# Optimization experiments

Hardware: AMD Instinct MI355X
Metric: run time of the kernel (lower is better)

The kernel has to match this reference:

```python
import jax, jax.numpy as jnp
import numpy as np

B, Q, HIST, HID, NH, D, BS, NBLK, NUMB = 8, 512, 1536, 4096, 32, 128, 64, 32, 256


def _rope(x, pos):
    # GPT-NeoX-style rotary used by Falcon: rotate_half over full head_dim.
    Dh = x.shape[-1]
    inv = 1.0 / (10000.0 ** (jnp.arange(0, Dh, 2, dtype=jnp.float32) / Dh))  # [D/2]
    ang = pos.astype(jnp.float32)[:, None] * inv[None, :]                    # [T, D/2]
    cos = jnp.concatenate([jnp.cos(ang), jnp.cos(ang)], -1)[None, :, None, :]
    sin = jnp.concatenate([jnp.sin(ang), jnp.sin(ang)], -1)[None, :, None, :]
    half = Dh // 2
    rot = jnp.concatenate([-x[..., half:], x[..., :half]], -1)
    return x * cos + rot * sin


def setup_inputs() -> dict:
    key = jax.random.key(0)
    ks = jax.random.split(key, 6)
    hidden_states = jax.random.normal(ks[0], (1, B * Q, HID), jnp.float32) * 0.02
    qkv_weight = jax.random.normal(ks[1], ((NH + 2) * D, HID), jnp.float32) * 0.02
    dense_weight = jax.random.normal(ks[2], (HID, NH * D), jnp.float32) * 0.02
    past_key = jax.random.normal(ks[3], (NUMB, BS, 1, D), jnp.float32) * 0.02
    past_value = jax.random.normal(ks[4], (NUMB, BS, 1, D), jnp.float32) * 0.02
    q_start_loc = (jnp.arange(B) * Q).astype(jnp.int32)
    q_seq_length = jnp.full((B,), Q, jnp.int32)
    history_lengths = jnp.full((B,), HIST, jnp.int32)
    # each sequence owns NBLK distinct cache blocks (shuffled block table)
    block_offsets = jax.random.permutation(ks[5], NUMB).reshape(B, NBLK).astype(jnp.int32)
    position_ids_1d = (history_lengths[:, None] + jnp.arange(Q, dtype=jnp.int32)[None, :]).reshape(-1)
    return dict(hidden_states=hidden_states, qkv_weight=qkv_weight, dense_weight=dense_weight,
                past_key=past_key, past_value=past_value, q_start_loc=q_start_loc,
                q_seq_length=q_seq_length, history_lengths=history_lengths,
                block_offsets=block_offsets, position_ids_1d=position_ids_1d)


def reference(hidden_states, qkv_weight, dense_weight, past_key, past_value,
              q_start_loc, q_seq_length, history_lengths, block_offsets, position_ids_1d):
    T = hidden_states.shape[1]
    Bn = block_offsets.shape[0]
    Qn = T // Bn
    Dh = past_key.shape[-1]
    BSz = past_key.shape[1]
    # fused QKV projection
    fused = hidden_states @ qkv_weight.T                      # [1, T, (NH+2)*D]
    NHh = fused.shape[-1] // Dh - 2
    qkv = fused.reshape(1, T, NHh + 2, Dh)
    q = qkv[:, :, :NHh]                                       # [1, T, NH, D]
    k = qkv[:, :, NHh:NHh + 1]                                 # [1, T, 1, D]
    v = qkv[:, :, NHh + 1:]                                    # [1, T, 1, D]
    # inline rotary embedding on q, k
    q = _rope(q, position_ids_1d)
    k = _rope(k, position_ids_1d)
    # fill_kv_cache: scatter new K/V into paged cache via block table
    seq_id = jnp.repeat(jnp.arange(Bn), Qn)                   # [T]
    pos = position_ids_1d.astype(jnp.int32)                   # absolute kv position
    blk = block_offsets[seq_id, pos // BSz]                   # [T] physical block id
    off = pos % BSz
    past_key = past_key.at[blk, off].set(k.reshape(T, 1, Dh))
    past_value = past_value.at[blk, off].set(v.reshape(T, 1, Dh))
    # paged_attention_fwd: gather per-sequence K/V from paged cache
    KVc = block_offsets.shape[1] * BSz                        # kv capacity == kv_len here
    kseq = past_key[block_offsets].reshape(Bn, KVc, Dh)       # [B, KV, D] (1 kv head squeezed)
    vseq = past_value[block_offsets].reshape(Bn, KVc, Dh)
    qb = q.reshape(Bn, Qn, NHh, Dh)
    scale = 1.0 / jnp.sqrt(jnp.float32(Dh))
    scores = jnp.einsum('bqhd,bkd->bhqk', qb, kseq) * scale   # [B, H, Q, KV]
    qpos = history_lengths[:, None] + jnp.arange(Qn)[None, :] # [B, Q]
    mask = jnp.arange(KVc)[None, None, :] <= qpos[:, :, None] # causal + length mask
    scores = jnp.where(mask[:, None, :, :], scores, jnp.float32(-1e30))
    attn = jax.nn.softmax(scores, axis=-1)
    out = jnp.einsum('bhqk,bkd->bqhd', attn, vseq)            # [B, Q, H, D]
    out = out.reshape(1, T, NHh * Dh)
    return out @ dense_weight.T                                # [1, T, hidden]
```

## Files before the change

### kernel.cpp

```cpp
#include <hip/hip_runtime.h>

typedef __attribute__((ext_vector_type(8))) short bf16x8;
typedef __attribute__((ext_vector_type(4))) float f32x4;
typedef __attribute__((ext_vector_type(16))) float f32x16;
typedef __attribute__((ext_vector_type(2))) unsigned int u32x2;

constexpr int B_ = 8, Q_ = 512, HIST_ = 1536, HID_ = 4096, NH_ = 32, D_ = 128;
constexpr int BS_ = 64, NBLK_ = 32;
constexpr int T_ = B_ * Q_;
constexpr int QKVN = (NH_ + 2) * D_;
constexpr int KVC = NBLK_ * BS_;

__device__ __forceinline__ unsigned short f2bf(float f) {
  union { float f; unsigned u; } v; v.f = f;
  unsigned r = v.u + 0x7FFFu + ((v.u >> 16) & 1u);
  return (unsigned short)(r >> 16);
}
__device__ __forceinline__ float bf2f(unsigned short s) {
  union { unsigned u; float f; } v; v.u = ((unsigned)s) << 16;
  return v.f;
}
__device__ __forceinline__ int cvtpk_bf16(float lo, float hi) {
  int r;
  asm("v_cvt_pk_bf16_f32 %0, %1, %2" : "=v"(r) : "v"(lo), "v"(hi));
  return r;
}

__global__ void k_conv3(const float* __restrict__ a, unsigned short* __restrict__ oa, int na,
                        const float* __restrict__ b2, unsigned short* __restrict__ ob, int nb,
                        const float* __restrict__ c3, unsigned short* __restrict__ oc, int nc) {
  int i = blockIdx.x * blockDim.x + threadIdx.x;
  const int stride = gridDim.x * blockDim.x;
  const int tot = na + nb + nc;
  for (; i < tot; i += stride) {
    const float* src; unsigned short* dst; int j = i;
    if (j < na) { src = a; dst = oa; }
    else if ((j -= na) < nb) { src = b2; dst = ob; }
    else { j -= nb; src = c3; dst = oc; }
    float4 v = reinterpret_cast<const float4*>(src)[j];
    ushort4 o;
    o.x = f2bf(v.x); o.y = f2bf(v.y); o.z = f2bf(v.z); o.w = f2bf(v.w);
    reinterpret_cast<ushort4*>(dst)[j] = o;
  }
}

#define LDA4(af, cur_, qq)                                                              \
  {                                                                                     \
    const unsigned short* a_t = sA + (cur_) * 16384;                                    \
    const int r0 = wr * 128 + (qq) * 32 + lr;                                           \
    const int r1 = r0 + 16;                                                             \
    af[0][0] = *(const bf16x8*)&a_t[r0 * 64 + ((lk ^ (r0 & 7)) << 3)];                  \
    af[0][1] = *(const bf16x8*)&a_t[r0 * 64 + (((4 + lk) ^ (r0 & 7)) << 3)];            \
    af[1][0] = *(const bf16x8*)&a_t[r1 * 64 + ((lk ^ (r1 & 7)) << 3)];                  \
    af[1][1] = *(const bf16x8*)&a_t[r1 * 64 + (((4 + lk) ^ (r1 & 7)) << 3)];            \
  }

#define LDB2(dst, cur_, nn)                                                             \
  {                                                                                     \
    const unsigned short* b_t = sB + (cur_) * 16384;                                    \
    const int rb = wc * 64 + (nn) * 16 + lr;                                            \
    dst[nn][0] = *(const bf16x8*)&b_t[rb * 64 + ((lk ^ (rb & 7)) << 3)];                \
    dst[nn][1] = *(const bf16x8*)&b_t[rb * 64 + (((4 + lk) ^ (rb & 7)) << 3)];          \
  }

#define MFMA16(qq, af, Bf)                                                              \
  __builtin_amdgcn_s_setprio(1);                                                        \
  acc[(qq)*2+0][0] = __builtin_amdgcn_mfma_f32_16x16x32_bf16(af[0][0], Bf[0][0], acc[(qq)*2+0][0], 0, 0, 0); \
  acc[(qq)*2+0][1] = __builtin_amdgcn_mfma_f32_16x16x32_bf16(af[0][0], Bf[1][0], acc[(qq)*2+0][1], 0, 0, 0); \
  acc[(qq)*2+0][2] = __builtin_amdgcn_mfma_f32_16x16x32_bf16(af[0][0], Bf[2][0], acc[(qq)*2+0][2], 0, 0, 0); \
  acc[(qq)*2+0][3] = __builtin_amdgcn_mfma_f32_16x16x32_bf16(af[0][0], Bf[3][0], acc[(qq)*2+0][3], 0, 0, 0); \
  acc[(qq)*2+1][0] = __builtin_amdgcn_mfma_f32_16x16x32_bf16(af[1][0], Bf[0][0], acc[(qq)*2+1][0], 0, 0, 0); \
  acc[(qq)*2+1][1] = __builtin_amdgcn_mfma_f32_16x16x32_bf16(af[1][0], Bf[1][0], acc[(qq)*2+1][1], 0, 0, 0); \
  acc[(qq)*2+1][2] = __builtin_amdgcn_mfma_f32_16x16x32_bf16(af[1][0], Bf[2][0], acc[(qq)*2+1][2], 0, 0, 0); \
  acc[(qq)*2+1][3] = __builtin_amdgcn_mfma_f32_16x16x32_bf16(af[1][0], Bf[3][0], acc[(qq)*2+1][3], 0, 0, 0); \
  acc[(qq)*2+0][0] = __builtin_amdgcn_mfma_f32_16x16x32_bf16(af[0][1], Bf[0][1], acc[(qq)*2+0][0], 0, 0, 0); \
  acc[(qq)*2+0][1] = __builtin_amdgcn_mfma_f32_16x16x32_bf16(af[0][1], Bf[1][1], acc[(qq)*2+0][1], 0, 0, 0); \
  acc[(qq)*2+0][2] = __builtin_amdgcn_mfma_f32_16x16x32_bf16(af[0][1], Bf[2][1], acc[(qq)*2+0][2], 0, 0, 0); \
  acc[(qq)*2+0][3] = __builtin_amdgcn_mfma_f32_16x16x32_bf16(af[0][1], Bf[3][1], acc[(qq)*2+0][3], 0, 0, 0); \
  acc[(qq)*2+1][0] = __builtin_amdgcn_mfma_f32_16x16x32_bf16(af[1][1], Bf[0][1], acc[(qq)*2+1][0], 0, 0, 0); \
  acc[(qq)*2+1][1] = __builtin_amdgcn_mfma_f32_16x16x32_bf16(af[1][1], Bf[1][1], acc[(qq)*2+1][1], 0, 0, 0); \
  acc[(qq)*2+1][2] = __builtin_amdgcn_mfma_f32_16x16x32_bf16(af[1][1], Bf[2][1], acc[(qq)*2+1][2], 0, 0, 0); \
  acc[(qq)*2+1][3] = __builtin_amdgcn_mfma_f32_16x16x32_bf16(af[1][1], Bf[3][1], acc[(qq)*2+1][3], 0, 0, 0); \
  __builtin_amdgcn_s_setprio(0);

#define SYNCPT                                                                          \
  asm volatile("s_waitcnt vmcnt(4)" ::: "memory");                                      \
  __builtin_amdgcn_s_barrier();                                                         \
  asm volatile("" ::: "memory");

#define TILE(t_, cur_, BCUR, BNEXT)                                                     \
  {                                                                                     \
    bf16x8 af[2][2];                                                                    \
    LDA4(af, cur_, 0);                                                                  \
    stage(A, m0, sA, (t_) + 1, 0);                                                      \
    MFMA16(0, af, BCUR);                                                                \
    LDA4(af, cur_, 1);                                                                  \
    stage(A, m0, sA, (t_) + 1, 1);                                                      \
    MFMA16(1, af, BCUR);                                                                \
    SYNCPT;                                                                             \
    LDA4(af, cur_, 2);                                                                  \
    LDB2(BNEXT, (cur_) ^ 1, 0); LDB2(BNEXT, (cur_) ^ 1, 1);                             \
    stage(Bm, n0, sB, (t_) + 2, 0);                                                     \
    MFMA16(2, af, BCUR);                                                                \
    LDA4(af, cur_, 3);                                                                  \
    LDB2(BNEXT, (cur_) ^ 1, 2); LDB2(BNEXT, (cur_) ^ 1, 3);                             \
    stage(Bm, n0, sB, (t_) + 2, 1);                                                     \
    MFMA16(3, af, BCUR);                                                                \
    SYNCPT;                                                                             \
  }

__global__ __launch_bounds__(512, 2) void k_gemm256(const unsigned short* __restrict__ A,
                          const unsigned short* __restrict__ Bm,
                          float* __restrict__ Cf, unsigned short* __restrict__ Cb,
                          int MB, int K, int ldc) {
  extern __shared__ unsigned short smem[];
  unsigned short* sA = smem;
  unsigned short* sB = smem + 32768;
  const int tid = threadIdx.x, lane = tid & 63, w = tid >> 6;
  const int wr = w >> 2, wc = w & 3;
  const int lr = lane & 15, lk = lane >> 4;

  const int nwg = gridDim.x, orig = blockIdx.x;
  const int q8 = nwg >> 3, r8 = nwg & 7, xcd = orig & 7;
  const int wg = (xcd < r8 ? xcd * (q8 + 1) : r8 * (q8 + 1) + (xcd - r8) * q8) + (orig >> 3);
  const int m0 = (wg % MB) * 256;
  const int n0 = (wg / MB) * 256;
  const int NT = K >> 6;

  f32x4 acc[8][4];
#pragma unroll
  for (int mf = 0; mf < 8; ++mf)
#pragma unroll
    for (int nf = 0; nf < 4; ++nf) acc[mf][nf] = f32x4{0.f, 0.f, 0.f, 0.f};

  auto stage = [&](const unsigned short* __restrict__ Mat, int rbase, unsigned short* regionBase,
                   int ts, int half) {
    const int di = ts < NT ? ts : NT - 1;
    const size_t k0 = (size_t)di << 6;
    char* hb = (char*)(regionBase + (ts & 1) * 16384 + half * 8192);
#pragma unroll
    for (int c = 0; c < 2; ++c) {
      const int ob = c * 8192 + (w << 10) + (lane << 4);
      const int row = ob >> 7;
      const int sl = ((ob >> 4) & 7) ^ (row & 7);
      const unsigned short* src = Mat + (size_t)(rbase + half * 128 + row) * K + k0 + sl * 8;
      __builtin_amdgcn_global_load_lds((const __attribute__((address_space(1))) void*)src,
          (__attribute__((address_space(3))) void*)(hb + c * 8192 + (w << 10)), 16, 0, 0);
    }
  };

  stage(A, m0, sA, 0, 0); stage(A, m0, sA, 0, 1);
  stage(Bm, n0, sB, 0, 0); stage(Bm, n0, sB, 0, 1);
  stage(Bm, n0, sB, 1, 0); stage(Bm, n0, sB, 1, 1);
  asm volatile("s_waitcnt vmcnt(4)" ::: "memory");
  __builtin_amdgcn_s_barrier();
  asm volatile("" ::: "memory");
  bf16x8 bX[4][2], bY[4][2];
  LDB2(bX, 0, 0); LDB2(bX, 0, 1); LDB2(bX, 0, 2); LDB2(bX, 0, 3);

  for (int t = 0; t < NT; t += 2) {
    TILE(t, 0, bX, bY)
    TILE(t + 1, 1, bY, bX)
  }
  asm volatile("s_waitcnt vmcnt(0)" ::: "memory");

#pragma unroll
  for (int mf = 0; mf < 8; ++mf)
#pragma unroll
    for (int nf = 0; nf < 4; ++nf)
#pragma unroll
      for (int j = 0; j < 4; ++j) {
        const int rr = m0 + wr * 128 + mf * 16 + lk * 4 + j;
        const int cc = n0 + wc * 64 + nf * 16 + lr;
        if (Cb) Cb[(size_t)rr * ldc + cc] = f2bf(acc[mf][nf][j]);
        else Cf[(size_t)rr * ldc + cc] = acc[mf][nf][j];
      }
}

__global__ void k_rope(const unsigned short* __restrict__ fused,
                       const int* __restrict__ pos_ids,
                       unsigned short* __restrict__ qb,
                       unsigned short* __restrict__ kseq,
                       unsigned short* __restrict__ vtg) {
  int t = blockIdx.x;
  int d = threadIdx.x;
  int b = t >> 9, q = t & 511;
  int pos = pos_ids[t];
  __shared__ float cs[64], sn[64];
  if (d < 64) {
    float inv = powf(10000.f, -(float)d * (1.f / 64.f));
    float ang = (float)pos * inv;
    cs[d] = cosf(ang);
    sn[d] = sinf(ang);
  }
  __syncthreads();
  const float scale = 0.1275174313836907f;
  float c = cs[d & 63], s = sn[d & 63];
  const unsigned short* row = fused + (size_t)t * QKVN;
#pragma unroll 4
  for (int h = 0; h < NH_; ++h) {
    float x = bf2f(row[h * D_ + d]);
    float xr = (d < 64) ? -bf2f(row[h * D_ + d + 64]) : bf2f(row[h * D_ + d - 64]);
    qb[(((size_t)(b * NH_ + h)) * Q_ + q) * D_ + d] = f2bf((x * c + xr * s) * scale);
  }
  {
    float x = bf2f(row[NH_ * D_ + d]);
    float xr = (d < 64) ? -bf2f(row[NH_ * D_ + d + 64]) : bf2f(row[NH_ * D_ + d - 64]);
    kseq[((size_t)b * KVC + pos) * D_ + d] = f2bf(x * c + xr * s);
  }
  vtg[((size_t)b * D_ + d) * KVC + pos] = row[(NH_ + 1) * D_ + d];
}

__global__ void k_gather(const float* __restrict__ pk, const float* __restrict__ pv,
                         const int* __restrict__ bo,
                         unsigned short* __restrict__ kseq, unsigned short* __restrict__ vtg) {
  __shared__ unsigned short vl[64 * 140];
  const int ptile = blockIdx.x;
  const int b = ptile / (HIST_ / 64);
  const int p0 = (ptile % (HIST_ / 64)) * 64;
  const int tid = threadIdx.x;
  const int blk = bo[b * NBLK_ + (p0 >> 6)];
#pragma unroll
  for (int c = 0; c < 8; ++c) {
    int u = c * 256 + tid;
    int p = u >> 5, d4 = u & 31;
    size_t src = ((size_t)blk * BS_ + p) * D_ + d4 * 4;
    float4 kv = *reinterpret_cast<const float4*>(pk + src);
    ushort4 ko;
    ko.x = f2bf(kv.x); ko.y = f2bf(kv.y); ko.z = f2bf(kv.z); ko.w = f2bf(kv.w);
    *reinterpret_cast<ushort4*>(kseq + ((size_t)b * KVC + p0 + p) * D_ + d4 * 4) = ko;
    float4 vv = *reinterpret_cast<const float4*>(pv + src);
    ushort4 vo;
    vo.x = f2bf(vv.x); vo.y = f2bf(vv.y); vo.z = f2bf(vv.z); vo.w = f2bf(vv.w);
    *reinterpret_cast<ushort4*>(&vl[p * 140 + d4 * 4]) = vo;
  }
  __syncthreads();
#pragma unroll
  for (int c = 0; c < 4; ++c) {
    int u = c * 256 + tid;
    int d = u >> 3, pg = u & 7;
    bf16x8 vv8;
#pragma unroll
    for (int i = 0; i < 8; ++i) vv8[i] = (short)vl[(pg * 8 + i) * 140 + d];
    *reinterpret_cast<bf16x8*>(vtg + ((size_t)b * D_ + d) * KVC + p0 + pg * 8) = vv8;
  }
}

__global__ __launch_bounds__(512, 2) void k_attn(const unsigned short* __restrict__ qb,
                       const unsigned short* __restrict__ kseq,
                       const unsigned short* __restrict__ vtg,
                       const int* __restrict__ histL,
                       unsigned short* __restrict__ outb) {
  __shared__ alignas(16) unsigned short kl[2][64 * 128];
  __shared__ alignas(16) unsigned short vt[2][128 * 64];
  const int qt = blockIdx.x, hp = blockIdx.y, b = blockIdx.z;
  const int tid = threadIdx.x, lane = tid & 63, w = tid >> 6;
  const int H = lane >> 5, q = lane & 31;
  const int h = hp * 8 + w;
  const int q0 = qt * 32;
  const int hist = histL[b];
  const unsigned short* kseq_b = kseq + (size_t)b * KVC * D_;
  const unsigned short* vtg_b  = vtg + (size_t)b * D_ * KVC;

  const unsigned short* qrow = qb + (((size_t)(b * NH_ + h)) * Q_ + q0 + q) * D_;
  bf16x8 aq[8];
#pragma unroll
  for (int ds = 0; ds < 8; ++ds)
    aq[ds] = *reinterpret_cast<const bf16x8*>(qrow + ds * 16 + H * 8);

  f32x16 o[4];
#pragma unroll
  for (int db = 0; db < 4; ++db)
#pragma unroll
    for (int r = 0; r < 16; ++r) o[db][r] = 0.f;
  float m = -1e30f, l = 0.f;

  const int ntiles = (hist + q0 + 32 + 63) >> 6;

  auto STAGE = [&](int bufi, int kv0) {
#pragma unroll
    for (int c = 0; c < 2; ++c) {
      int ob = c * 8192 + tid * 16;
      int row = ob >> 8;
      int sp = (ob >> 4) & 15;
      const unsigned short* src = kseq_b + (size_t)(kv0 + row) * D_ + (((sp ^ (row & 15)) << 3));
      __builtin_amdgcn_global_load_lds((const __attribute__((address_space(1))) void*)src,
          (__attribute__((address_space(3))) void*)(&kl[bufi][c * 4096 + w * 512]), 16, 0, 0);
    }
#pragma unroll
    for (int c = 0; c < 2; ++c) {
      int ob = c * 8192 + tid * 16;
      int row = ob >> 7;
      int sp = (ob >> 4) & 7;
      const unsigned short* src = vtg_b + (size_t)row * KVC + kv0 + (((sp ^ (row & 7)) << 3));
      __builtin_amdgcn_global_load_lds((const __attribute__((address_space(1))) void*)src,
          (__attribute__((address_space(3))) void*)(&vt[bufi][c * 4096 + w * 512]), 16, 0, 0);
    }
  };

  STAGE(0, 0);
  __syncthreads();

  for (int it = 0; it < ntiles; ++it) {
    const int cur = it & 1;
    if (it + 1 < ntiles) STAGE(cur ^ 1, (it + 1) * 64);
    const unsigned short* kb = kl[cur];
    const unsigned short* vb = vt[cur];

    f32x16 s0 = f32x16{0.f,0.f,0.f,0.f,0.f,0.f,0.f,0.f,0.f,0.f,0.f,0.f,0.f,0.f,0.f,0.f};
    f32x16 s1 = s0;
#pragma unroll
    for (int ds = 0; ds < 8; ++ds) {
      const int sl = ((2 * ds + H) ^ (q & 15)) << 3;
      bf16x8 k0 = *reinterpret_cast<const bf16x8*>(kb + q * 128 + sl);
      bf16x8 k1 = *reinterpret_cast<const bf16x8*>(kb + (32 + q) * 128 + sl);
      s0 = __builtin_amdgcn_mfma_f32_32x32x16_bf16(k0, aq[ds], s0, 0, 0, 0);
      s1 = __builtin_amdgcn_mfma_f32_32x32x16_bf16(k1, aq[ds], s1, 0, 0, 0);
    }

    if (it == ntiles - 1) {
      const int limit = hist + q0 + q - it * 64 - 4 * H;
#pragma unroll
      for (int r = 0; r < 16; ++r) {
        const int koff = (r & 3) + 8 * ((r >> 2) & 1) + 16 * (r >> 3);
        if (koff > limit) s0[r] = -1e30f;
        if (32 + koff > limit) s1[r] = -1e30f;
      }
    }

    float px[8];
#pragma unroll
    for (int j = 0; j < 8; ++j) {
      float t01 = fmaxf(s0[2 * j], s0[2 * j + 1]);
      px[j] = fmaxf(fmaxf(t01, s1[2 * j]), s1[2 * j + 1]);
    }
    float pa = fmaxf(fmaxf(px[0], px[1]), px[2]);
    float pb2 = fmaxf(fmaxf(px[3], px[4]), px[5]);
    float pmax = fmaxf(fmaxf(pa, pb2), fmaxf(px[6], px[7]));
    pmax = fmaxf(pmax, __shfl_xor(pmax, 32));
    if (__any(pmax > m + 11.54f)) {
      float mn = fmaxf(m, pmax);
      float al = exp2f(m - mn);
      m = mn;
      l *= al;
#pragma unroll
      for (int db = 0; db < 4; ++db)
#pragma unroll
        for (int r = 0; r < 16; ++r) o[db][r] *= al;
    }
#pragma unroll
    for (int r = 0; r < 16; ++r) s0[r] = exp2f(s0[r] - m);
#pragma unroll
    for (int r = 0; r < 16; ++r) s1[r] = exp2f(s1[r] - m);
    float rsum[8];
#pragma unroll
    for (int j = 0; j < 8; ++j)
      rsum[j] = (s0[2 * j] + s0[2 * j + 1]) + (s1[2 * j] + s1[2 * j + 1]);
    float rs = ((rsum[0] + rsum[1]) + (rsum[2] + rsum[3])) + ((rsum[4] + rsum[5]) + (rsum[6] + rsum[7]));
    rs += __shfl_xor(rs, 32);
    l += rs;

#pragma unroll
    for (int s = 0; s < 4; ++s) {
      float p0, p1, p2, p3, p4, p5, p6, p7;
      if (s == 0)      { p0=s0[0];p1=s0[1];p2=s0[2];p3=s0[3];p4=s0[4];p5=s0[5];p6=s0[6];p7=s0[7]; }
      else if (s == 1) { p0=s0[8];p1=s0[9];p2=s0[10];p3=s0[11];p4=s0[12];p5=s0[13];p6=s0[14];p7=s0[15]; }
      else if (s == 2) { p0=s1[0];p1=s1[1];p2=s1[2];p3=s1[3];p4=s1[4];p5=s1[5];p6=s1[6];p7=s1[7]; }
      else             { p0=s1[8];p1=s1[9];p2=s1[10];p3=s1[11];p4=s1[12];p5=s1[13];p6=s1[14];p7=s1[15]; }
      int c01 = cvtpk_bf16(p0, p1);
      int c23 = cvtpk_bf16(p2, p3);
      int c45 = cvtpk_bf16(p4, p5);
      int c67 = cvtpk_bf16(p6, p7);
      u32x2 rA = __builtin_amdgcn_permlane32_swap(c01, c45, false, false);
      u32x2 rB = __builtin_amdgcn_permlane32_swap(c23, c67, false, false);
      union { unsigned wds[4]; bf16x8 v; } uu;
      uu.wds[0] = rA[0]; uu.wds[1] = rB[0]; uu.wds[2] = rA[1]; uu.wds[3] = rB[1];
#pragma unroll
      for (int db = 0; db < 4; ++db) {
        const int row = db * 32 + q;
        bf16x8 vf = *reinterpret_cast<const bf16x8*>(vb + row * 64 + ((((2 * s + H) ^ (row & 7))) << 3));
        o[db] = __builtin_amdgcn_mfma_f32_32x32x16_bf16(vf, uu.v, o[db], 0, 0, 0);
      }
    }
    __syncthreads();
  }

  const float il = 1.f / l;
  unsigned short* orow = outb + (size_t)(b * Q_ + q0 + q) * (NH_ * D_) + h * D_;
#pragma unroll
  for (int db = 0; db < 4; ++db)
#pragma unroll
    for (int rr = 0; rr < 4; ++rr) {
      ushort4 st;
      st.x = f2bf(o[db][rr * 4 + 0] * il);
      st.y = f2bf(o[db][rr * 4 + 1] * il);
      st.z = f2bf(o[db][rr * 4 + 2] * il);
      st.w = f2bf(o[db][rr * 4 + 3] * il);
      *reinterpret_cast<ushort4*>(orow + db * 32 + rr * 8 + 4 * H) = st;
    }
}

extern "C" void kernel_launch(void* const* d_in, const int* in_sizes, int n_in,
                              void* d_out, int out_size, void* d_ws, size_t ws_size,
                              hipStream_t stream) {
  const float* hidden = (const float*)d_in[0];
  const float* qkvw   = (const float*)d_in[1];
  const float* densew = (const float*)d_in[2];
  const float* pk     = (const float*)d_in[3];
  const float* pv     = (const float*)d_in[4];
  const int* histL    = (const int*)d_in[7];
  const int* bo       = (const int*)d_in[8];
  const int* posids   = (const int*)d_in[9];
  float* out = (float*)d_out;

  char* ws = (char*)d_ws;
  unsigned short* ws_hidden = (unsigned short*)(ws);
  unsigned short* ws_wq     = (unsigned short*)(ws + 33554432);
  unsigned short* ws_wd     = (unsigned short*)(ws + 69206016);
  unsigned short* ws_fused  = (unsigned short*)(ws + 102760448);
  unsigned short* ws_q      = (unsigned short*)(ws + 138412032);
  unsigned short* ws_k      = (unsigned short*)(ws + 171966464);
  unsigned short* ws_vt     = (unsigned short*)(ws + 176160768);
  unsigned short* ws_attn   = ws_hidden;

  k_conv3<<<2048, 256, 0, stream>>>(hidden, ws_hidden, T_ * HID_ / 4,
                                    qkvw, ws_wq, QKVN * HID_ / 4,
                                    densew, ws_wd, HID_ * HID_ / 4);
  k_gemm256<<<dim3((T_ / 256) * (QKVN / 256)), 512, 131072, stream>>>(
      ws_hidden, ws_wq, nullptr, ws_fused, T_ / 256, HID_, QKVN);
  k_rope<<<T_, 128, 0, stream>>>(ws_fused, posids, ws_q, ws_k, ws_vt);
  k_gather<<<B_ * (HIST_ / 64), 256, 0, stream>>>(pk, pv, bo, ws_k, ws_vt);
  dim3 ga(Q_ / 32, NH_ / 8, B_);
  k_attn<<<ga, 512, 0, stream>>>(ws_q, ws_k, ws_vt, histL, ws_attn);
  k_gemm256<<<dim3((T_ / 256) * (HID_ / 256)), 512, 131072, stream>>>(
      ws_attn, ws_wd, out, nullptr, T_ / 256, HID_, HID_);
}
```

Baseline: 539.2 us.

## Fuse query RoPE into attention prologue and precompute cos/sin table

Removes the separate rotated-Q buffer by applying rotary embedding and the softmax scale to Q inside the attention kernel as it loads Q from the fused QKV output. A new small kernel precomputes per-token cos/sin tables, used by both the K rope kernel and attention. This removes a full write and re-read of the Q tensor, at the cost of strided Q loads from the fused buffer and extra prologue math and table reads in attention.

```diff
diff --git a/kernel.cpp b/kernel.cpp
--- a/kernel.cpp
+++ b/kernel.cpp
@@ -42,6 +42,14 @@
     o.x = f2bf(v.x); o.y = f2bf(v.y); o.z = f2bf(v.z); o.w = f2bf(v.w);
     reinterpret_cast<ushort4*>(dst)[j] = o;
   }
+}
+
+__global__ void k_tab(const int* __restrict__ posids, float* __restrict__ cs, float* __restrict__ sn) {
+  const int t = blockIdx.x, d = threadIdx.x;
+  const float inv = powf(10000.f, -(float)d * (1.f / 64.f));
+  const float ang = (float)posids[t] * inv;
+  cs[t * 64 + d] = cosf(ang);
+  sn[t * 64 + d] = sinf(ang);
 }
 
 #define LDA4(af, cur_, qq)                                                              \
@@ -177,37 +185,20 @@
       }
 }
 
-__global__ void k_rope(const unsigned short* __restrict__ fused,
-                       const int* __restrict__ pos_ids,
-                       unsigned short* __restrict__ qb,
-                       unsigned short* __restrict__ kseq,
-                       unsigned short* __restrict__ vtg) {
-  int t = blockIdx.x;
-  int d = threadIdx.x;
-  int b = t >> 9, q = t & 511;
-  int pos = pos_ids[t];
-  __shared__ float cs[64], sn[64];
-  if (d < 64) {
-    float inv = powf(10000.f, -(float)d * (1.f / 64.f));
-    float ang = (float)pos * inv;
-    cs[d] = cosf(ang);
-    sn[d] = sinf(ang);
-  }
-  __syncthreads();
-  const float scale = 0.1275174313836907f;
-  float c = cs[d & 63], s = sn[d & 63];
+__global__ void k_ropekv(const unsigned short* __restrict__ fused,
+                         const int* __restrict__ pos_ids,
+                         const float* __restrict__ csT, const float* __restrict__ snT,
+                         unsigned short* __restrict__ kseq,
+                         unsigned short* __restrict__ vtg) {
+  const int t = blockIdx.x;
+  const int d = threadIdx.x;
+  const int b = t >> 9;
+  const int pos = pos_ids[t];
+  const float c = csT[t * 64 + (d & 63)], s = snT[t * 64 + (d & 63)];
   const unsigned short* row = fused + (size_t)t * QKVN;
-#pragma unroll 4
-  for (int h = 0; h < NH_; ++h) {
-    float x = bf2f(row[h * D_ + d]);
-    float xr = (d < 64) ? -bf2f(row[h * D_ + d + 64]) : bf2f(row[h * D_ + d - 64]);
-    qb[(((size_t)(b * NH_ + h)) * Q_ + q) * D_ + d] = f2bf((x * c + xr * s) * scale);
-  }
-  {
-    float x = bf2f(row[NH_ * D_ + d]);
-    float xr = (d < 64) ? -bf2f(row[NH_ * D_ + d + 64]) : bf2f(row[NH_ * D_ + d - 64]);
-    kseq[((size_t)b * KVC + pos) * D_ + d] = f2bf(x * c + xr * s);
-  }
+  const float x = bf2f(row[NH_ * D_ + d]);
+  const float xr = (d < 64) ? -bf2f(row[NH_ * D_ + d + 64]) : bf2f(row[NH_ * D_ + d - 64]);
+  kseq[((size_t)b * KVC + pos) * D_ + d] = f2bf(x * c + xr * s);
   vtg[((size_t)b * D_ + d) * KVC + pos] = row[(NH_ + 1) * D_ + d];
 }
 
@@ -246,7 +237,8 @@
   }
 }
 
-__global__ __launch_bounds__(512, 2) void k_attn(const unsigned short* __restrict__ qb,
+__global__ __launch_bounds__(512, 2) void k_attn(const unsigned short* __restrict__ fused,
+                       const float* __restrict__ csT, const float* __restrict__ snT,
                        const unsigned short* __restrict__ kseq,
                        const unsigned short* __restrict__ vtg,
                        const int* __restrict__ histL,
@@ -262,11 +254,36 @@
   const unsigned short* kseq_b = kseq + (size_t)b * KVC * D_;
   const unsigned short* vtg_b  = vtg + (size_t)b * D_ * KVC;
 
-  const unsigned short* qrow = qb + (((size_t)(b * NH_ + h)) * Q_ + q0 + q) * D_;
+  const int trow = b * Q_ + q0 + q;
+  const unsigned short* qrow = fused + (size_t)trow * QKVN + h * D_;
+  const float* csr = csT + trow * 64;
+  const float* snr = snT + trow * 64;
   bf16x8 aq[8];
 #pragma unroll
   for (int ds = 0; ds < 8; ++ds)
     aq[ds] = *reinterpret_cast<const bf16x8*>(qrow + ds * 16 + H * 8);
+  {
+    const float qsc = 0.1275174313836907f;
+#pragma unroll
+    for (int ds = 0; ds < 4; ++ds) {
+      const int dh0 = ds * 16 + H * 8;
+      float4 ca = *reinterpret_cast<const float4*>(csr + dh0);
+      float4 cb = *reinterpret_cast<const float4*>(csr + dh0 + 4);
+      float4 sa = *reinterpret_cast<const float4*>(snr + dh0);
+      float4 sb = *reinterpret_cast<const float4*>(snr + dh0 + 4);
+      const float cl[8] = {ca.x, ca.y, ca.z, ca.w, cb.x, cb.y, cb.z, cb.w};
+      const float sl[8] = {sa.x, sa.y, sa.z, sa.w, sb.x, sb.y, sb.z, sb.w};
+      bf16x8 lo = aq[ds], hi = aq[ds + 4];
+#pragma unroll
+      for (int j = 0; j < 8; ++j) {
+        const float xl = bf2f((unsigned short)lo[j]);
+        const float xh = bf2f((unsigned short)hi[j]);
+        lo[j] = (short)f2bf((xl * cl[j] - xh * sl[j]) * qsc);
+        hi[j] = (short)f2bf((xh * cl[j] + xl * sl[j]) * qsc);
+      }
+      aq[ds] = lo; aq[ds + 4] = hi;
+    }
+  }
 
   f32x16 o[4];
 #pragma unroll
@@ -418,20 +435,22 @@
   unsigned short* ws_wq     = (unsigned short*)(ws + 33554432);
   unsigned short* ws_wd     = (unsigned short*)(ws + 69206016);
   unsigned short* ws_fused  = (unsigned short*)(ws + 102760448);
-  unsigned short* ws_q      = (unsigned short*)(ws + 138412032);
-  unsigned short* ws_k      = (unsigned short*)(ws + 171966464);
-  unsigned short* ws_vt     = (unsigned short*)(ws + 176160768);
+  float* ws_cs              = (float*)(ws + 138412032);
+  float* ws_sn              = (float*)(ws + 139460608);
+  unsigned short* ws_k      = (unsigned short*)(ws + 140509184);
+  unsigned short* ws_vt     = (unsigned short*)(ws + 144703488);
   unsigned short* ws_attn   = ws_hidden;
 
   k_conv3<<<2048, 256, 0, stream>>>(hidden, ws_hidden, T_ * HID_ / 4,
                                     qkvw, ws_wq, QKVN * HID_ / 4,
                                     densew, ws_wd, HID_ * HID_ / 4);
+  k_tab<<<T_, 64, 0, stream>>>(posids, ws_cs, ws_sn);
   k_gemm256<<<dim3((T_ / 256) * (QKVN / 256)), 512, 131072, stream>>>(
       ws_hidden, ws_wq, nullptr, ws_fused, T_ / 256, HID_, QKVN);
-  k_rope<<<T_, 128, 0, stream>>>(ws_fused, posids, ws_q, ws_k, ws_vt);
+  k_ropekv<<<T_, 128, 0, stream>>>(ws_fused, posids, ws_cs, ws_sn, ws_k, ws_vt);
   k_gather<<<B_ * (HIST_ / 64), 256, 0, stream>>>(pk, pv, bo, ws_k, ws_vt);
   dim3 ga(Q_ / 32, NH_ / 8, B_);
-  k_attn<<<ga, 512, 0, stream>>>(ws_q, ws_k, ws_vt, histL, ws_attn);
+  k_attn<<<ga, 512, 0, stream>>>(ws_fused, ws_cs, ws_sn, ws_k, ws_vt, histL, ws_attn);
   k_gemm256<<<dim3((T_ / 256) * (HID_ / 256)), 512, 131072, stream>>>(
       ws_attn, ws_wd, out, nullptr, T_ / 256, HID_, HID_);
 }
```

After: 536.2 us. No clear change (-0.6%).
